# Optimization experiments

Hardware: AMD Instinct MI355X
Metric: run time of the kernel (lower is better)

The kernel has to match this reference:

```python
import jax, jax.numpy as jnp
import numpy as np
from functools import partial

H = 768
E = 1536
B = 4
L = 4096

def layer_norm(x, g, b, eps=1e-5):
    mu = jnp.mean(x, axis=-1, keepdims=True)
    var = jnp.mean((x - mu) ** 2, axis=-1, keepdims=True)
    return (x - mu) * jax.lax.rsqrt(var + eps) * g + b

def l2_normalize(x, eps=1e-12):
    n = jnp.sqrt(jnp.sum(x * x, axis=-1, keepdims=True))
    return x / jnp.maximum(n, eps)

def dw_conv(x, w):
    # x: [B, L, E], w: [E, 1, 3] depthwise kernel (torch Conv1d groups=E layout)
    y = jax.lax.conv_general_dilated(
        x.transpose(0, 2, 1), w, window_strides=(1,), padding=[(1, 1)],
        dimension_numbers=('NCH', 'OIH', 'NCH'), feature_group_count=E)
    return y.transpose(0, 2, 1)

def setup_inputs() -> dict:
    key = jax.random.key(0)
    ks = jax.random.split(key, 12)
    d = {}
    d['x'] = jax.random.normal(ks[0], (B, L, H), jnp.float32)
    d['ln1_g'] = jnp.ones((H,), jnp.float32)
    d['ln1_b'] = jnp.zeros((H,), jnp.float32)
    d['ln2_g'] = jnp.ones((E,), jnp.float32)
    d['ln2_b'] = jnp.zeros((E,), jnp.float32)
    d['W_in'] = 0.02 * jax.random.normal(ks[1], (3 * E, H), jnp.float32)
    d['b_in'] = jnp.zeros((3 * E,), jnp.float32)
    d['W_beta'] = jnp.zeros((E, H), jnp.float32)  # torch init: constant 0
    d['b_beta'] = jnp.ones((E,), jnp.float32)     # torch init: constant 1
    d['W_out'] = 0.02 * jax.random.normal(ks[2], (H, E), jnp.float32)
    d['b_out'] = jnp.zeros((H,), jnp.float32)
    d['W1'] = 0.02 * jax.random.normal(ks[3], (4 * H, H), jnp.float32)
    d['b1'] = jnp.zeros((4 * H,), jnp.float32)
    d['W2'] = 0.02 * jax.random.normal(ks[4], (H, 4 * H), jnp.float32)
    d['b2'] = jnp.zeros((H,), jnp.float32)
    d['conv_w'] = jax.random.normal(ks[5], (E, 1, 3), jnp.float32) / jnp.sqrt(3.0)
    d['attn_scale'] = jnp.ones((1,), jnp.float32)
    return d

def reference(x, ln1_g, ln1_b, ln2_g, ln2_b, W_in, b_in, W_beta, b_beta,
              W_out, b_out, W1, b1, W2, b2, conv_w, attn_scale):
    shortcut = x
    xn = layer_norm(x, ln1_g, ln1_b)
    qkv = xn @ W_in.T + b_in
    q, k, v = jnp.split(qkv, 3, axis=-1)
    q = jax.nn.silu(q)
    k = jax.nn.silu(k)
    v = jax.nn.gelu(v, approximate=False)
    q = l2_normalize(q) + 0.1 * k
    k = l2_normalize(k) + 0.1 * q
    q = dw_conv(q, conv_w)
    k = dw_conv(k, conv_w)
    v = dw_conv(v, conv_w)
    beta = jax.nn.sigmoid(xn @ W_beta.T + b_beta) * 0.9 + 0.1
    # initial state is zero, so v_old = 0 and v_new = beta * v (same math as torch code)
    v_new = beta * v                                   # [B, L, E]
    state = jnp.einsum('ble,blf->bef', v_new, k)       # v_new^T @ k : [B, E, E]
    out = jnp.einsum('blf,bef->ble', q, state)         # q @ state^T
    out = out * attn_scale
    out = layer_norm(out, ln2_g, ln2_b)
    out = out @ W_out.T + b_out
    x = shortcut + out
    h = layer_norm(x, ln1_g, ln1_b)
    h = jax.nn.gelu(h @ W1.T + b1, approximate=False) @ W2.T + b2
    return x + h
```

## Files before the change

kernel.cpp:

```cpp
#include <hip/hip_runtime.h>
#include <hip/hip_bf16.h>
#include <cstdint>
#include <cstddef>

using bf16_t = __hip_bfloat16;
typedef __bf16 bf16x8 __attribute__((ext_vector_type(8)));
typedef __bf16 bf16x4 __attribute__((ext_vector_type(4)));
typedef float f32x4 __attribute__((ext_vector_type(4)));

#define DEVI static __device__ __forceinline__

DEVI float b2f(bf16_t v) { return __bfloat162float(v); }

DEVI float fsigmoid(float x) { return 1.0f / (1.0f + __expf(-x)); }
DEVI float fsilu(float x) { return x * fsigmoid(x); }

DEVI float ferf(float x) {
    const float ax = fabsf(x);
    const float t = 1.0f / fmaf(0.3275911f, ax, 1.0f);
    float p = fmaf(1.061405429f, t, -1.453152027f);
    p = fmaf(p, t, 1.421413741f);
    p = fmaf(p, t, -0.284496736f);
    p = fmaf(p, t, 0.254829592f);
    p = p * t * __expf(-ax * ax);
    return copysignf(1.0f - p, x);
}
DEVI float fgelu(float x) { return 0.5f * x * (1.0f + ferf(x * 0.70710678118654752440f)); }

DEVI void g2l16(const bf16_t* g, bf16_t* l) {
    __builtin_amdgcn_global_load_lds(
        (const __attribute__((address_space(1))) void*)g,
        (__attribute__((address_space(3))) void*)l,
        16, 0, 0);
}

template<int ACT, bool RESID, bool OUTBF, bool QKVSPLIT>
__global__ __launch_bounds__(256) void gemm_nt(
    const bf16_t* __restrict__ A, const bf16_t* __restrict__ B,
    void* __restrict__ Cout, const float* __restrict__ bias,
    const float* __restrict__ resid,
    float* __restrict__ normq, float* __restrict__ normk,
    int M, int N, int K, long long sA, long long sB, long long sC)
{
    __shared__ bf16_t As[128 * 64];
    __shared__ bf16_t Bs[128 * 64];

    const int t  = threadIdx.x;
    const int w  = t >> 6;
    const int ln = t & 63;
    const long long bz = blockIdx.z;
    A += bz * sA;
    B += bz * sB;
    const long long cbase = QKVSPLIT ? 0 : bz * sC;

    const int m0 = blockIdx.y * 128;
    const int n0 = blockIdx.x * 128;
    const int wm = (w >> 1) * 64;
    const int wn = (w & 1) * 64;

    f32x4 acc[4][4] = {};

    const int sr = ln >> 3;
    const int sc = (ln & 7) ^ sr;
    const bf16_t* Ap = A + (size_t)(m0 + w * 32 + sr) * K + sc * 8;
    const bf16_t* Bp = B + (size_t)(n0 + w * 32 + sr) * K + sc * 8;
    bf16_t* ldsA = &As[(w * 32) * 64];
    bf16_t* ldsB = &Bs[(w * 32) * 64];

    const int fr = ln & 15;
    const int qd = ln >> 4;
    int roA[4], roB[4];
#pragma unroll
    for (int i = 0; i < 4; ++i) {
        roA[i] = (wm + i * 16 + fr) * 64;
        roB[i] = (wn + i * 16 + fr) * 64;
    }
    const int so0 = ((qd)     ^ (fr & 7)) * 8;
    const int so1 = ((4 + qd) ^ (fr & 7)) * 8;

    for (int k0 = 0; k0 < K; k0 += 64) {
#pragma unroll
        for (int i = 0; i < 4; ++i) {
            g2l16(Ap + (size_t)(i * 8) * K, ldsA + (i * 8) * 64);
            g2l16(Bp + (size_t)(i * 8) * K, ldsB + (i * 8) * 64);
        }
        Ap += 64; Bp += 64;
        __syncthreads();

        bf16x8 af[4], bfr[4];
#pragma unroll
        for (int i = 0; i < 4; ++i) {
            af[i]  = *(const bf16x8*)&As[roA[i] + so0];
            bfr[i] = *(const bf16x8*)&Bs[roB[i] + so0];
        }
#pragma unroll
        for (int mi = 0; mi < 4; ++mi)
#pragma unroll
            for (int ni = 0; ni < 4; ++ni)
                acc[mi][ni] = __builtin_amdgcn_mfma_f32_16x16x32_bf16(
                    bfr[ni], af[mi], acc[mi][ni], 0, 0, 0);
#pragma unroll
        for (int i = 0; i < 4; ++i) {
            af[i]  = *(const bf16x8*)&As[roA[i] + so1];
            bfr[i] = *(const bf16x8*)&Bs[roB[i] + so1];
        }
#pragma unroll
        for (int mi = 0; mi < 4; ++mi)
#pragma unroll
            for (int ni = 0; ni < 4; ++ni)
                acc[mi][ni] = __builtin_amdgcn_mfma_f32_16x16x32_bf16(
                    bfr[ni], af[mi], acc[mi][ni], 0, 0, 0);
        __syncthreads();
    }

    const int rb = qd * 4;
    const int seg = QKVSPLIT ? (n0 / 1536) : 0;
    f32x4 bias4[4];
#pragma unroll
    for (int ni = 0; ni < 4; ++ni) {
        f32x4 z = {};
        bias4[ni] = bias ? *(const f32x4*)&bias[n0 + wn + ni * 16 + rb] : z;
    }
#pragma unroll
    for (int mi = 0; mi < 4; ++mi) {
        const int row = m0 + wm + mi * 16 + fr;
        float s2 = 0.f;
#pragma unroll
        for (int ni = 0; ni < 4; ++ni) {
            const int col0 = n0 + wn + ni * 16 + rb;
            f32x4 v = acc[mi][ni] + bias4[ni];
            if constexpr (ACT == 1) {
#pragma unroll
                for (int r = 0; r < 4; ++r) v[r] = fgelu(v[r]);
            }
            if constexpr (ACT == 3) {
                if (seg <= 1) {
#pragma unroll
                    for (int r = 0; r < 4; ++r) v[r] = fsilu(v[r]);
                    s2 += v[0]*v[0] + v[1]*v[1] + v[2]*v[2] + v[3]*v[3];
                } else if (seg == 2) {
#pragma unroll
                    for (int r = 0; r < 4; ++r) v[r] = fgelu(v[r]);
                } else {
#pragma unroll
                    for (int r = 0; r < 4; ++r) v[r] = fsigmoid(v[r]) * 0.9f + 0.1f;
                }
            }
            long long off;
            if constexpr (QKVSPLIT) {
                off = (long long)seg * sC + (long long)row * 1536
                    + (col0 - seg * 1536);
            } else {
                off = cbase + (long long)row * N + col0;
            }
            if constexpr (RESID) v += *(const f32x4*)&resid[off];
            if constexpr (OUTBF) {
                bf16x4 o;
#pragma unroll
                for (int r = 0; r < 4; ++r) o[r] = (__bf16)v[r];
                *(bf16x4*)((bf16_t*)Cout + off) = o;
            } else {
                *(f32x4*)((float*)Cout + off) = v;
            }
        }
        if constexpr (ACT == 3) {
            if (seg <= 1) {
                s2 += __shfl_xor(s2, 16, 64);
                s2 += __shfl_xor(s2, 32, 64);
                if (qd == 0)
                    atomicAdd((seg == 0 ? normq : normk) + row, s2);
            }
        }
    }
}

template<int NT>
__global__ __launch_bounds__(NT) void ln_v4(
    const float* __restrict__ x, const float* __restrict__ g,
    const float* __restrict__ b, bf16_t* __restrict__ out)
{
    constexpr int n = NT * 4;
    constexpr int NW = NT / 64;
    const int row = blockIdx.x, t = threadIdx.x;
    f32x4 v = *(const f32x4*)&x[(size_t)row * n + t * 4];
    float s  = v[0] + v[1] + v[2] + v[3];
    float ss = v[0]*v[0] + v[1]*v[1] + v[2]*v[2] + v[3]*v[3];
#pragma unroll
    for (int m = 32; m; m >>= 1) { s += __shfl_xor(s, m, 64); ss += __shfl_xor(ss, m, 64); }
    __shared__ float red[2 * NW];
    const int w = t >> 6;
    if ((t & 63) == 0) { red[w] = s; red[NW + w] = ss; }
    __syncthreads();
    s = 0.f; ss = 0.f;
#pragma unroll
    for (int i = 0; i < NW; ++i) { s += red[i]; ss += red[NW + i]; }
    const float mean = s / n;
    const float rstd = rsqrtf(ss / n - mean * mean + 1e-5f);
    const f32x4 gv = *(const f32x4*)&g[t * 4];
    const f32x4 bv = *(const f32x4*)&b[t * 4];
    bf16x4 o;
#pragma unroll
    for (int r = 0; r < 4; ++r)
        o[r] = (__bf16)((v[r] - mean) * rstd * gv[r] + bv[r]);
    *(bf16x4*)&out[(size_t)row * n + t * 4] = o;
}

__global__ __launch_bounds__(192) void ln_bf16_1536(
    const bf16_t* __restrict__ x, const float* __restrict__ g,
    const float* __restrict__ b, bf16_t* __restrict__ out,
    const float* __restrict__ scale_ptr)
{
    const int row = blockIdx.x, t = threadIdx.x;
    const float scale = scale_ptr[0];
    const bf16x8 x8 = *(const bf16x8*)&x[(size_t)row * 1536 + t * 8];
    float v[8];
    float s = 0.f, ss = 0.f;
#pragma unroll
    for (int i = 0; i < 8; ++i) {
        v[i] = (float)x8[i] * scale;
        s += v[i]; ss += v[i] * v[i];
    }
#pragma unroll
    for (int m = 32; m; m >>= 1) { s += __shfl_xor(s, m, 64); ss += __shfl_xor(ss, m, 64); }
    __shared__ float red[6];
    const int w = t >> 6;
    if ((t & 63) == 0) { red[w] = s; red[3 + w] = ss; }
    __syncthreads();
    s  = red[0] + red[1] + red[2];
    ss = red[3] + red[4] + red[5];
    const float mean = s / 1536.f;
    const float rstd = rsqrtf(ss / 1536.f - mean * mean + 1e-5f);
    const f32x4 g0 = *(const f32x4*)&g[t * 8];
    const f32x4 g1 = *(const f32x4*)&g[t * 8 + 4];
    const f32x4 b0 = *(const f32x4*)&b[t * 8];
    const f32x4 b1 = *(const f32x4*)&b[t * 8 + 4];
    bf16x8 o;
#pragma unroll
    for (int r = 0; r < 4; ++r) {
        o[r]     = (__bf16)((v[r]     - mean) * rstd * g0[r] + b0[r]);
        o[r + 4] = (__bf16)((v[r + 4] - mean) * rstd * g1[r] + b1[r]);
    }
    *(bf16x8*)&out[(size_t)row * 1536 + t * 8] = o;
}

__global__ __launch_bounds__(256) void ac_qk(
    const bf16_t* __restrict__ qs, const bf16_t* __restrict__ ks,
    const float* __restrict__ nq, const float* __restrict__ nk,
    bf16_t* __restrict__ qc, bf16_t* __restrict__ kT,
    const float* __restrict__ cw)
{
    constexpr int L = 4096, E = 1536;
    const int b = blockIdx.z;
    const int e0 = blockIdx.x * 64, l0 = blockIdx.y * 64;
    const int t = threadIdx.x;
    const int e = e0 + (t & 15) * 4;
    const int lbase = l0 + (t >> 4) * 4;
    const size_t rowL = (size_t)b * L;

    float w0[4], w1[4], w2[4];
#pragma unroll
    for (int i = 0; i < 4; ++i) {
        w0[i] = cw[(e + i) * 3 + 0];
        w1[i] = cw[(e + i) * 3 + 1];
        w2[i] = cw[(e + i) * 3 + 2];
    }

    float sq[6][4], sk[6][4];
#pragma unroll
    for (int j = 0; j < 6; ++j) {
        const int l = lbase - 1 + j;
        if (l < 0 || l >= L) {
#pragma unroll
            for (int i = 0; i < 4; ++i) { sq[j][i] = 0.f; sk[j][i] = 0.f; }
            continue;
        }
        const size_t off = (rowL + l) * E + e;
        const bf16x4 q4 = *(const bf16x4*)&qs[off];
        const bf16x4 k4 = *(const bf16x4*)&ks[off];
        const float rq = 1.0f / fmaxf(sqrtf(nq[rowL + l]), 1e-12f);
        const float rk = 1.0f / fmaxf(sqrtf(nk[rowL + l]), 1e-12f);
#pragma unroll
        for (int i = 0; i < 4; ++i) {
            const float q1 = (float)q4[i] * rq + 0.1f * (float)k4[i];
            const float k1 = (float)k4[i] * rk + 0.1f * q1;
            sq[j][i] = q1; sk[j][i] = k1;
        }
    }

#pragma unroll
    for (int j = 0; j < 4; ++j) {
        bf16x4 oq;
#pragma unroll
        for (int i = 0; i < 4; ++i)
            oq[i] = (__bf16)(w0[i] * sq[j][i] + w1[i] * sq[j + 1][i] + w2[i] * sq[j + 2][i]);
        *(bf16x4*)&qc[(rowL + lbase + j) * E + e] = oq;
    }
#pragma unroll
    for (int i = 0; i < 4; ++i) {
        bf16x4 ok;
#pragma unroll
        for (int j = 0; j < 4; ++j)
            ok[j] = (__bf16)(w0[i] * sk[j][i] + w1[i] * sk[j + 1][i] + w2[i] * sk[j + 2][i]);
        *(bf16x4*)&kT[((size_t)b * E + e + i) * L + lbase] = ok;
    }
}

__global__ __launch_bounds__(256) void ac_v(
    const bf16_t* __restrict__ vg, const bf16_t* __restrict__ beta,
    bf16_t* __restrict__ vT, const float* __restrict__ cw)
{
    constexpr int L = 4096, E = 1536;
    const int b = blockIdx.z;
    const int e0 = blockIdx.x * 64, l0 = blockIdx.y * 64;
    const int t = threadIdx.x;
    const int e = e0 + (t & 15) * 4;
    const int lbase = l0 + (t >> 4) * 4;
    const size_t rowL = (size_t)b * L;

    float w0[4], w1[4], w2[4];
#pragma unroll
    for (int i = 0; i < 4; ++i) {
        w0[i] = cw[(e + i) * 3 + 0];
        w1[i] = cw[(e + i) * 3 + 1];
        w2[i] = cw[(e + i) * 3 + 2];
    }

    float s[6][4];
#pragma unroll
    for (int j = 0; j < 6; ++j) {
        const int l = lbase - 1 + j;
        if (l < 0 || l >= L) {
#pragma unroll
            for (int i = 0; i < 4; ++i) s[j][i] = 0.f;
            continue;
        }
        const bf16x4 v4 = *(const bf16x4*)&vg[(rowL + l) * E + e];
#pragma unroll
        for (int i = 0; i < 4; ++i) s[j][i] = (float)v4[i];
    }

    float o[4][4];
#pragma unroll
    for (int j = 0; j < 4; ++j) {
        const bf16x4 b4 = *(const bf16x4*)&beta[(rowL + lbase + j) * E + e];
#pragma unroll
        for (int i = 0; i < 4; ++i)
            o[j][i] = (w0[i] * s[j][i] + w1[i] * s[j + 1][i] + w2[i] * s[j + 2][i])
                      * (float)b4[i];
    }
#pragma unroll
    for (int i = 0; i < 4; ++i) {
        bf16x4 ov;
#pragma unroll
        for (int j = 0; j < 4; ++j) ov[j] = (__bf16)o[j][i];
        *(bf16x4*)&vT[((size_t)b * E + e + i) * L + lbase] = ov;
    }
}

__global__ __launch_bounds__(256) void prep1(
    const float* __restrict__ Win, const float* __restrict__ Wbeta,
    const float* __restrict__ bin, const float* __restrict__ bbeta,
    bf16_t* __restrict__ Wcat, float* __restrict__ bcat)
{
    constexpr int nWin4 = 3 * 1536 * 768 / 4;
    constexpr int nWb4  = 1536 * 768 / 4;
    const int i = blockIdx.x * 256 + threadIdx.x;
    if (i < nWin4) {
        const f32x4 v = ((const f32x4*)Win)[i];
        bf16x4 o;
#pragma unroll
        for (int r = 0; r < 4; ++r) o[r] = (__bf16)v[r];
        ((bf16x4*)Wcat)[i] = o;
    } else if (i < nWin4 + nWb4) {
        const f32x4 v = ((const f32x4*)Wbeta)[i - nWin4];
        bf16x4 o;
#pragma unroll
        for (int r = 0; r < 4; ++r) o[r] = (__bf16)v[r];
        ((bf16x4*)Wcat)[i] = o;
    } else {
        const int j = i - nWin4 - nWb4;
        ((f32x4*)bcat)[j] = (j < 1152) ? ((const f32x4*)bin)[j]
                                       : ((const f32x4*)bbeta)[j - 1152];
    }
}

__global__ __launch_bounds__(256) void prep2(
    const float* __restrict__ Wout, const float* __restrict__ W1,
    const float* __restrict__ W2, bf16_t* __restrict__ dst)
{
    constexpr int n0 = 768 * 1536 / 4;
    constexpr int n1 = n0 + 3072 * 768 / 4;
    const int i = blockIdx.x * 256 + threadIdx.x;
    const float* src;
    int j;
    if (i < n0)      { src = Wout; j = i; }
    else if (i < n1) { src = W1;   j = i - n0; }
    else             { src = W2;   j = i - n1; }
    const f32x4 v = ((const f32x4*)src)[j];
    bf16x4 o;
#pragma unroll
    for (int r = 0; r < 4; ++r) o[r] = (__bf16)v[r];
    ((bf16x4*)dst)[i] = o;
}

__global__ void diag_ws(float* o, float v) { o[threadIdx.x] = v; }


extern "C" void kernel_launch(void* const* d_in, const int* in_sizes, int n_in,
                              void* d_out, int out_size, void* d_ws, size_t ws_size,
                              hipStream_t stream)
{
    constexpr int B = 4, L = 4096, H = 768, E = 1536;
    constexpr int T = B * L;
    constexpr size_t SEGE = (size_t)T * E;
    constexpr size_t S    = SEGE * 2;
    constexpr size_t o_bcat  = 5 * S;
    constexpr size_t o_norms = o_bcat + 6144 * 4;
    constexpr size_t WS_NEED = o_norms + (size_t)T * 8;

    const float* x       = (const float*)d_in[0];
    const float* ln1_g   = (const float*)d_in[1];
    const float* ln1_b   = (const float*)d_in[2];
    const float* ln2_g   = (const float*)d_in[3];
    const float* ln2_b   = (const float*)d_in[4];
    const float* W_in    = (const float*)d_in[5];
    const float* b_in    = (const float*)d_in[6];
    const float* W_beta  = (const float*)d_in[7];
    const float* b_beta  = (const float*)d_in[8];
    const float* W_out   = (const float*)d_in[9];
    const float* b_out   = (const float*)d_in[10];
    const float* W1      = (const float*)d_in[11];
    const float* b1      = (const float*)d_in[12];
    const float* W2      = (const float*)d_in[13];
    const float* b2      = (const float*)d_in[14];
    const float* conv_w  = (const float*)d_in[15];
    const float* attn_sc = (const float*)d_in[16];

    if (ws_size < WS_NEED) {
        diag_ws<<<1, 256, 0, stream>>>((float*)d_out,
                                       10000.0f + (float)(ws_size >> 20));
        return;
    }

    char* ws = (char*)d_ws;
    bf16_t* slotA = (bf16_t*)(ws + 0 * S);
    bf16_t* slotB = (bf16_t*)(ws + 1 * S);
    bf16_t* slotC = (bf16_t*)(ws + 2 * S);
    bf16_t* slotD = (bf16_t*)(ws + 3 * S);
    bf16_t* slotE = (bf16_t*)(ws + 4 * S);
    float*  bcat  = (float*)(ws + o_bcat);
    float*  nq    = (float*)(ws + o_norms);
    float*  nk    = nq + T;

    bf16_t* Wcat = slotE;
    bf16_t* xn   = (bf16_t*)((char*)slotE + (size_t)6144 * H * 2);

    bf16_t* vT    = slotE;
    bf16_t* kT    = slotC;
    bf16_t* qc    = slotD;
    bf16_t* state = slotA;
    bf16_t* WoutB = (bf16_t*)((char*)slotA + (size_t)20 * 1024 * 1024);
    bf16_t* W1B   = WoutB + (size_t)H * E;
    bf16_t* W2B   = W1B + (size_t)4 * H * H;
    bf16_t* attn  = slotB;
    bf16_t* ln2o  = slotE;
    float*  x2    = (float*)slotC;
    bf16_t* xn2   = slotB;
    bf16_t* h1    = slotD;

    hipMemsetAsync(nq, 0, (size_t)T * 2 * sizeof(float), stream);
    prep1<<<4614, 256, 0, stream>>>(W_in, W_beta, b_in, b_beta, Wcat, bcat);

    ln_v4<192><<<T, 192, 0, stream>>>(x, ln1_g, ln1_b, xn);

    gemm_nt<3, false, true, true><<<dim3(6144 / 128, T / 128, 1), 256, 0, stream>>>(
        xn, Wcat, slotA, bcat, nullptr, nq, nk, T, 6144, H, 0, 0, (long long)SEGE);

    ac_v <<<dim3(E / 64, L / 64, B), 256, 0, stream>>>(slotC, slotD, vT, conv_w);
    ac_qk<<<dim3(E / 64, L / 64, B), 256, 0, stream>>>(slotA, slotB, nq, nk, qc, kT, conv_w);

    prep2<<<5760, 256, 0, stream>>>(W_out, W1, W2, WoutB);

    gemm_nt<0, false, true, false><<<dim3(E / 128, E / 128, B), 256, 0, stream>>>(
        vT, kT, state, nullptr, nullptr, nullptr, nullptr, E, E, L,
        (long long)E * L, (long long)E * L, (long long)E * E);

    gemm_nt<0, false, true, false><<<dim3(E / 128, L / 128, B), 256, 0, stream>>>(
        qc, state, attn, nullptr, nullptr, nullptr, nullptr, L, E, E,
        (long long)L * E, (long long)E * E, (long long)L * E);

    ln_bf16_1536<<<T, 192, 0, stream>>>(attn, ln2_g, ln2_b, ln2o, attn_sc);

    gemm_nt<0, true, false, false><<<dim3(H / 128, T / 128, 1), 256, 0, stream>>>(
        ln2o, WoutB, x2, b_out, x, nullptr, nullptr, T, H, E, 0, 0, 0);

    ln_v4<192><<<T, 192, 0, stream>>>(x2, ln1_g, ln1_b, xn2);

    gemm_nt<1, false, true, false><<<dim3(4 * H / 128, T / 128, 1), 256, 0, stream>>>(
        xn2, W1B, h1, b1, nullptr, nullptr, nullptr, T, 4 * H, H, 0, 0, 0);

    gemm_nt<0, true, false, false><<<dim3(H / 128, T / 128, 1), 256, 0, stream>>>(
        h1, W2B, (float*)d_out, b2, x2, nullptr, nullptr, T, H, 4 * H, 0, 0, 0);
}
```

Baseline: 1.066 ms.

## Add 256x256 double-buffered pipelined GEMM kernel for large-N GEMMs

Adds a new 512-thread GEMM kernel with 256x256 output tiles, double-buffered LDS, and interleaved global-to-LDS prefetch placed between MFMA phases, using s_setprio and sched barriers. It is used for the QKV projection, the q@state GEMM and the FFN up-projection. The goal is more reuse per loaded tile and overlap of memory loads with MFMA work. In exchange it uses much more LDS and registers per block, and the grid has fewer blocks, which may underfill the CUs on the smaller GEMMs.

After: 1.028 ms. 1.04x faster.

```diff
diff --git a/kernel.cpp b/kernel.cpp
--- a/kernel.cpp
+++ b/kernel.cpp
@@ -34,6 +34,10 @@
         16, 0, 0);
 }
 
+DEVI f32x4 mfma16(bf16x8 a, bf16x8 b, f32x4 c) {
+    return __builtin_amdgcn_mfma_f32_16x16x32_bf16(a, b, c, 0, 0, 0);
+}
+
 template<int ACT, bool RESID, bool OUTBF, bool QKVSPLIT>
 __global__ __launch_bounds__(256) void gemm_nt(
     const bf16_t* __restrict__ A, const bf16_t* __restrict__ B,
@@ -97,8 +101,7 @@
         for (int mi = 0; mi < 4; ++mi)
 #pragma unroll
             for (int ni = 0; ni < 4; ++ni)
-                acc[mi][ni] = __builtin_amdgcn_mfma_f32_16x16x32_bf16(
-                    bfr[ni], af[mi], acc[mi][ni], 0, 0, 0);
+                acc[mi][ni] = mfma16(bfr[ni], af[mi], acc[mi][ni]);
 #pragma unroll
         for (int i = 0; i < 4; ++i) {
             af[i]  = *(const bf16x8*)&As[roA[i] + so1];
@@ -108,8 +111,7 @@
         for (int mi = 0; mi < 4; ++mi)
 #pragma unroll
             for (int ni = 0; ni < 4; ++ni)
-                acc[mi][ni] = __builtin_amdgcn_mfma_f32_16x16x32_bf16(
-                    bfr[ni], af[mi], acc[mi][ni], 0, 0, 0);
+                acc[mi][ni] = mfma16(bfr[ni], af[mi], acc[mi][ni]);
         __syncthreads();
     }
 
@@ -128,6 +130,256 @@
 #pragma unroll
         for (int ni = 0; ni < 4; ++ni) {
             const int col0 = n0 + wn + ni * 16 + rb;
+            f32x4 v = acc[mi][ni] + bias4[ni];
+            if constexpr (ACT == 1) {
+#pragma unroll
+                for (int r = 0; r < 4; ++r) v[r] = fgelu(v[r]);
+            }
+            if constexpr (ACT == 3) {
+                if (seg <= 1) {
+#pragma unroll
+                    for (int r = 0; r < 4; ++r) v[r] = fsilu(v[r]);
+                    s2 += v[0]*v[0] + v[1]*v[1] + v[2]*v[2] + v[3]*v[3];
+                } else if (seg == 2) {
+#pragma unroll
+                    for (int r = 0; r < 4; ++r) v[r] = fgelu(v[r]);
+                } else {
+#pragma unroll
+                    for (int r = 0; r < 4; ++r) v[r] = fsigmoid(v[r]) * 0.9f + 0.1f;
+                }
+            }
+            long long off;
+            if constexpr (QKVSPLIT) {
+                off = (long long)seg * sC + (long long)row * 1536
+                    + (col0 - seg * 1536);
+            } else {
+                off = cbase + (long long)row * N + col0;
+            }
+            if constexpr (RESID) v += *(const f32x4*)&resid[off];
+            if constexpr (OUTBF) {
+                bf16x4 o;
+#pragma unroll
+                for (int r = 0; r < 4; ++r) o[r] = (__bf16)v[r];
+                *(bf16x4*)((bf16_t*)Cout + off) = o;
+            } else {
+                *(f32x4*)((float*)Cout + off) = v;
+            }
+        }
+        if constexpr (ACT == 3) {
+            if (seg <= 1) {
+                s2 += __shfl_xor(s2, 16, 64);
+                s2 += __shfl_xor(s2, 32, 64);
+                if (qd == 0)
+                    atomicAdd((seg == 0 ? normq : normk) + row, s2);
+            }
+        }
+    }
+}
+
+template<int ACT, bool RESID, bool OUTBF, bool QKVSPLIT>
+__global__ __launch_bounds__(512) void gemm256(
+    const bf16_t* __restrict__ A, const bf16_t* __restrict__ B,
+    void* __restrict__ Cout, const float* __restrict__ bias,
+    const float* __restrict__ resid,
+    float* __restrict__ normq, float* __restrict__ normk,
+    int M, int N, int K, long long sA, long long sB, long long sC)
+{
+    __shared__ bf16_t As[2][256 * 64];
+    __shared__ bf16_t Bs[2][256 * 64];
+
+    const int t  = threadIdx.x;
+    const int w  = t >> 6;
+    const int ln = t & 63;
+    const int wr = w >> 2;
+    const int wc = w & 3;
+    const long long bz = blockIdx.z;
+    A += bz * sA;
+    B += bz * sB;
+    const long long cbase = QKVSPLIT ? 0 : bz * sC;
+
+    const int m0 = blockIdx.y * 256;
+    const int n0 = blockIdx.x * 256;
+
+    const int fr = ln & 15;
+    const int qd = ln >> 4;
+    const int sr = ln >> 3;
+    const int scx = ((ln & 7) ^ sr) * 8;
+
+    const bf16_t* gA[2];
+    const bf16_t* gB[2];
+    int lA[2], lB[2];
+#pragma unroll
+    for (int i = 0; i < 2; ++i) {
+        const int b  = w * 2 + i;
+        const int rA = ((b >> 3) << 7) + ((b & 7) << 3);
+        const int rB = ((b >> 2) << 6) + ((b & 3) << 3);
+        gA[i] = A + (size_t)(m0 + rA + sr) * K + scx;
+        gB[i] = B + (size_t)(n0 + rB + sr) * K + scx;
+        lA[i] = rA * 64;
+        lB[i] = rB * 64;
+    }
+    const size_t K64 = (size_t)K * 64;
+    const size_t K32 = (size_t)K * 32;
+    const int NT = K >> 6;
+
+    const int ck0 = ((qd)     ^ (fr & 7)) * 8;
+    const int ck1 = ((4 + qd) ^ (fr & 7)) * 8;
+    const int raB = (wr * 128 + fr) * 64;
+    const int rbB = (wc * 64  + fr) * 64;
+
+    f32x4 acc[8][4] = {};
+
+#pragma unroll
+    for (int i = 0; i < 2; ++i) {
+        g2l16(gA[i],       &As[0][lA[i]]);
+        g2l16(gA[i] + K64, &As[0][lA[i] + 4096]);
+        g2l16(gB[i],       &Bs[0][lB[i]]);
+        g2l16(gB[i] + K32, &Bs[0][lB[i] + 2048]);
+    }
+#pragma unroll
+    for (int i = 0; i < 2; ++i) {
+        g2l16(gB[i] + 64,       &Bs[1][lB[i]]);
+        g2l16(gA[i] + K64 + 64, &As[1][lA[i] + 4096]);
+    }
+    asm volatile("s_waitcnt vmcnt(4)" ::: "memory");
+    __builtin_amdgcn_sched_barrier(0);
+    __builtin_amdgcn_s_barrier();
+
+    for (int u = 0; u < NT; ++u) {
+        const int bs = u & 1;
+        const bf16_t* Ac = As[bs];
+        const bf16_t* Bc = Bs[bs];
+        bf16_t* An  = As[bs ^ 1];
+        bf16_t* Bn  = Bs[bs ^ 1];
+        bf16_t* Acw = As[bs];
+        bf16_t* Bcw = Bs[bs];
+        const size_t kc1 = (size_t)(u + 1) * 64;
+        const size_t kc2 = (size_t)(u + 2) * 64;
+        const bool p1 = (u + 1) < NT;
+        const bool p2 = (u + 2) < NT;
+
+        bf16x8 a0[4][2], a1[4][2], bq0[2][2], bq1[2][2];
+
+#pragma unroll
+        for (int mi = 0; mi < 4; ++mi) {
+            a0[mi][0] = *(const bf16x8*)&Ac[raB + mi * 1024 + ck0];
+            a0[mi][1] = *(const bf16x8*)&Ac[raB + mi * 1024 + ck1];
+        }
+#pragma unroll
+        for (int ni = 0; ni < 2; ++ni) {
+            bq0[ni][0] = *(const bf16x8*)&Bc[rbB + ni * 1024 + ck0];
+            bq0[ni][1] = *(const bf16x8*)&Bc[rbB + ni * 1024 + ck1];
+        }
+        if (p1) {
+            g2l16(gA[0] + kc1, &An[lA[0]]);
+            g2l16(gA[1] + kc1, &An[lA[1]]);
+        }
+        __builtin_amdgcn_s_barrier();
+        asm volatile("s_waitcnt lgkmcnt(0)" ::: "memory");
+        __builtin_amdgcn_sched_barrier(0);
+        __builtin_amdgcn_s_setprio(1);
+#pragma unroll
+        for (int mi = 0; mi < 4; ++mi)
+#pragma unroll
+            for (int ni = 0; ni < 2; ++ni) {
+                acc[mi][ni] = mfma16(bq0[ni][0], a0[mi][0], acc[mi][ni]);
+                acc[mi][ni] = mfma16(bq0[ni][1], a0[mi][1], acc[mi][ni]);
+            }
+        __builtin_amdgcn_s_setprio(0);
+        __builtin_amdgcn_sched_barrier(0);
+        __builtin_amdgcn_s_barrier();
+
+#pragma unroll
+        for (int mi = 0; mi < 4; ++mi) {
+            a1[mi][0] = *(const bf16x8*)&Ac[raB + 4096 + mi * 1024 + ck0];
+            a1[mi][1] = *(const bf16x8*)&Ac[raB + 4096 + mi * 1024 + ck1];
+        }
+        if (p1) {
+            g2l16(gB[0] + K32 + kc1, &Bn[lB[0] + 2048]);
+            g2l16(gB[1] + K32 + kc1, &Bn[lB[1] + 2048]);
+        }
+        __builtin_amdgcn_s_barrier();
+        asm volatile("s_waitcnt lgkmcnt(0)" ::: "memory");
+        __builtin_amdgcn_sched_barrier(0);
+        __builtin_amdgcn_s_setprio(1);
+#pragma unroll
+        for (int mi = 0; mi < 4; ++mi)
+#pragma unroll
+            for (int ni = 0; ni < 2; ++ni) {
+                acc[mi + 4][ni] = mfma16(bq0[ni][0], a1[mi][0], acc[mi + 4][ni]);
+                acc[mi + 4][ni] = mfma16(bq0[ni][1], a1[mi][1], acc[mi + 4][ni]);
+            }
+        __builtin_amdgcn_s_setprio(0);
+        __builtin_amdgcn_sched_barrier(0);
+        __builtin_amdgcn_s_barrier();
+
+#pragma unroll
+        for (int ni = 0; ni < 2; ++ni) {
+            bq1[ni][0] = *(const bf16x8*)&Bc[rbB + 2048 + ni * 1024 + ck0];
+            bq1[ni][1] = *(const bf16x8*)&Bc[rbB + 2048 + ni * 1024 + ck1];
+        }
+        if (p2) {
+            g2l16(gB[0] + kc2, &Bcw[lB[0]]);
+            g2l16(gB[1] + kc2, &Bcw[lB[1]]);
+        }
+        __builtin_amdgcn_s_barrier();
+        asm volatile("s_waitcnt lgkmcnt(0)" ::: "memory");
+        __builtin_amdgcn_sched_barrier(0);
+        __builtin_amdgcn_s_setprio(1);
+#pragma unroll
+        for (int mi = 0; mi < 4; ++mi)
+#pragma unroll
+            for (int ni = 0; ni < 2; ++ni) {
+                acc[mi + 4][ni + 2] = mfma16(bq1[ni][0], a1[mi][0], acc[mi + 4][ni + 2]);
+                acc[mi + 4][ni + 2] = mfma16(bq1[ni][1], a1[mi][1], acc[mi + 4][ni + 2]);
+            }
+        __builtin_amdgcn_s_setprio(0);
+        __builtin_amdgcn_sched_barrier(0);
+        __builtin_amdgcn_s_barrier();
+
+#pragma unroll
+        for (int mi = 0; mi < 4; ++mi) {
+            a0[mi][0] = *(const bf16x8*)&Ac[raB + mi * 1024 + ck0];
+            a0[mi][1] = *(const bf16x8*)&Ac[raB + mi * 1024 + ck1];
+        }
+        if (p2) {
+            g2l16(gA[0] + K64 + kc2, &Acw[lA[0] + 4096]);
+            g2l16(gA[1] + K64 + kc2, &Acw[lA[1] + 4096]);
+        }
+        __builtin_amdgcn_s_barrier();
+        asm volatile("s_waitcnt lgkmcnt(0)" ::: "memory");
+        __builtin_amdgcn_sched_barrier(0);
+        __builtin_amdgcn_s_setprio(1);
+#pragma unroll
+        for (int mi = 0; mi < 4; ++mi)
+#pragma unroll
+            for (int ni = 0; ni < 2; ++ni) {
+                acc[mi][ni + 2] = mfma16(bq1[ni][0], a0[mi][0], acc[mi][ni + 2]);
+                acc[mi][ni + 2] = mfma16(bq1[ni][1], a0[mi][1], acc[mi][ni + 2]);
+            }
+        __builtin_amdgcn_s_setprio(0);
+        __builtin_amdgcn_sched_barrier(0);
+        if (p2) asm volatile("s_waitcnt vmcnt(4)" ::: "memory");
+        else    asm volatile("s_waitcnt vmcnt(0)" ::: "memory");
+        __builtin_amdgcn_sched_barrier(0);
+        __builtin_amdgcn_s_barrier();
+    }
+
+    const int rb = qd * 4;
+    const int seg = QKVSPLIT ? (n0 / 1536) : 0;
+    f32x4 bias4[4];
+#pragma unroll
+    for (int ni = 0; ni < 4; ++ni) {
+        f32x4 z = {};
+        bias4[ni] = bias ? *(const f32x4*)&bias[n0 + wc * 64 + ni * 16 + rb] : z;
+    }
+#pragma unroll
+    for (int mi = 0; mi < 8; ++mi) {
+        const int row = m0 + wr * 128 + mi * 16 + fr;
+        float s2 = 0.f;
+#pragma unroll
+        for (int ni = 0; ni < 4; ++ni) {
+            const int col0 = n0 + wc * 64 + ni * 16 + rb;
             f32x4 v = acc[mi][ni] + bias4[ni];
             if constexpr (ACT == 1) {
 #pragma unroll
@@ -473,7 +725,7 @@
 
     ln_v4<192><<<T, 192, 0, stream>>>(x, ln1_g, ln1_b, xn);
 
-    gemm_nt<3, false, true, true><<<dim3(6144 / 128, T / 128, 1), 256, 0, stream>>>(
+    gemm256<3, false, true, true><<<dim3(6144 / 256, T / 256, 1), 512, 0, stream>>>(
         xn, Wcat, slotA, bcat, nullptr, nq, nk, T, 6144, H, 0, 0, (long long)SEGE);
 
     ac_v <<<dim3(E / 64, L / 64, B), 256, 0, stream>>>(slotC, slotD, vT, conv_w);
@@ -485,7 +737,7 @@
         vT, kT, state, nullptr, nullptr, nullptr, nullptr, E, E, L,
         (long long)E * L, (long long)E * L, (long long)E * E);
 
-    gemm_nt<0, false, true, false><<<dim3(E / 128, L / 128, B), 256, 0, stream>>>(
+    gemm256<0, false, true, false><<<dim3(E / 256, L / 256, B), 512, 0, stream>>>(
         qc, state, attn, nullptr, nullptr, nullptr, nullptr, L, E, E,
         (long long)L * E, (long long)E * E, (long long)L * E);
 
@@ -496,7 +748,7 @@
 
     ln_v4<192><<<T, 192, 0, stream>>>(x2, ln1_g, ln1_b, xn2);
 
-    gemm_nt<1, false, true, false><<<dim3(4 * H / 128, T / 128, 1), 256, 0, stream>>>(
+    gemm256<1, false, true, false><<<dim3(4 * H / 256, T / 256, 1), 512, 0, stream>>>(
         xn2, W1B, h1, b1, nullptr, nullptr, nullptr, T, 4 * H, H, 0, 0, 0);
 
     gemm_nt<0, true, false, false><<<dim3(H / 128, T / 128, 1), 256, 0, stream>>>(
```
